# Kernel tuning notes

Hardware: AMD Instinct MI355X
Metric: run time of the kernel (lower is better)

## Reference

```python
import jax, jax.numpy as jnp
import numpy as np

B, C, T = 8, 16, 1024
DM, DI, DS, DR, DC, L = 128, 256, 16, 8, 4, 4  # d_model, d_inner=2*d_model, d_state, dt_rank=d_model//16, d_conv, n_layers


def setup_inputs() -> dict:
    key = jax.random.key(0)
    ks = jax.random.split(key, 12)
    n = jax.random.normal
    s = 0.02
    A_init = jnp.log(jnp.arange(1, DS + 1, dtype=jnp.float32))  # S4D-real init
    return {
        "eeg_input": n(ks[0], (B, C, T), jnp.float32),
        "Win": n(ks[1], (C, DM)) * s, "b_in": jnp.zeros((DM,)),
        "ln_w": jnp.ones((L, DM)), "ln_b": jnp.zeros((L, DM)),
        "in_w": n(ks[2], (L, 2, DM, 2 * DI)) * s,
        "conv_w": n(ks[3], (L, 2, DI, DC)) * s, "conv_b": jnp.zeros((L, 2, DI)),
        "xp_w": n(ks[4], (L, 2, DI, DR + 2 * DS)) * s,
        "dt_w": n(ks[5], (L, 2, DR, DI)) * s, "dt_b": jnp.full((L, 2, DI), -4.6),  # softplus(-4.6) ~ 0.01
        "A_log": jnp.tile(A_init, (L, 2, DI, 1)), "Dp": jnp.ones((L, 2, DI)),
        "out_w": n(ks[6], (L, 2, DI, DM)) * s, "out_b": jnp.zeros((L, 2, DM)),
        "cls_ln_w": jnp.ones((DM,)), "cls_ln_b": jnp.zeros((DM,)),
        "W1": n(ks[7], (DM, DM // 2)) * s, "b1": jnp.zeros((DM // 2,)),
        "W2": n(ks[8], (DM // 2, 1)) * s, "b2": jnp.zeros((1,)),
    }


def _ln(x, w, b):
    m = x.mean(-1, keepdims=True)
    v = ((x - m) ** 2).mean(-1, keepdims=True)
    return (x - m) * jax.lax.rsqrt(v + 1e-5) * w + b


def _mamba(u, in_w, conv_w, conv_b, xp_w, dt_w, dt_b, A_log, Dp, out_w, out_b):
    # u: (B, T, DM)
    xz = u @ in_w                              # (B, T, 2*DI)
    x, z = jnp.split(xz, 2, axis=-1)
    # causal depthwise conv along time
    xc = jnp.transpose(x, (0, 2, 1))           # (B, DI, T)
    xc = jax.lax.conv_general_dilated(
        xc, conv_w[:, None, :], (1,), [(DC - 1, 0)],
        dimension_numbers=("NCH", "OIH", "NCH"), feature_group_count=DI,
    ) + conv_b[None, :, None]
    x = jax.nn.silu(jnp.transpose(xc, (0, 2, 1)))  # (B, T, DI)
    xdbl = x @ xp_w                            # (B, T, DR+2*DS)
    dt, Bss, Css = jnp.split(xdbl, [DR, DR + DS], axis=-1)
    delta = jax.nn.softplus(dt @ dt_w + dt_b)  # (B, T, DI)
    A = -jnp.exp(A_log)                        # (DI, DS)
    dA = jnp.exp(delta[..., None] * A)                       # (B, T, DI, DS)
    dBu = delta[..., None] * Bss[:, :, None, :] * x[..., None]  # (B, T, DI, DS)

    def step(h, inputs):
        dA_t, dBu_t, C_t = inputs
        h = dA_t * h + dBu_t                   # (B, DI, DS)
        y = jnp.einsum("bds,bs->bd", h, C_t)
        return h, y

    h0 = jnp.zeros((u.shape[0], DI, DS), u.dtype)
    _, ys = jax.lax.scan(step, h0, (jnp.swapaxes(dA, 0, 1), jnp.swapaxes(dBu, 0, 1), jnp.swapaxes(Css, 0, 1)))
    y = jnp.swapaxes(ys, 0, 1) + Dp * x        # (B, T, DI)
    y = y * jax.nn.silu(z)
    return y @ out_w + out_b


def reference(eeg_input, Win, b_in, ln_w, ln_b, in_w, conv_w, conv_b, xp_w, dt_w, dt_b,
              A_log, Dp, out_w, out_b, cls_ln_w, cls_ln_b, W1, b1, W2, b2):
    h = jnp.transpose(eeg_input, (0, 2, 1)) @ Win + b_in  # (B, T, DM)
    for l in range(L):
        xn = _ln(h, ln_w[l], ln_b[l])
        yf = _mamba(xn, in_w[l, 0], conv_w[l, 0], conv_b[l, 0], xp_w[l, 0], dt_w[l, 0],
                    dt_b[l, 0], A_log[l, 0], Dp[l, 0], out_w[l, 0], out_b[l, 0])
        yb = _mamba(xn[:, ::-1], in_w[l, 1], conv_w[l, 1], conv_b[l, 1], xp_w[l, 1], dt_w[l, 1],
                    dt_b[l, 1], A_log[l, 1], Dp[l, 1], out_w[l, 1], out_b[l, 1])[:, ::-1]
        h = h + yf + yb  # residual; dropout is identity in eval
    pooled = h.mean(axis=1)                    # (B, DM)
    p = _ln(pooled, cls_ln_w, cls_ln_b)
    p = jax.nn.gelu(p @ W1 + b1)
    return p @ W2 + b2                         # (B, 1)
```

## Files before the change

### kernel.cpp

```cpp
#include <hip/hip_runtime.h>
#include <hip/hip_bf16.h>

#define NB 8
#define NC 16
#define NT 1024
#define DM 128
#define DI 256
#define DS 16
#define DR 8
#define DC 4
#define NL 4
#define NCHUNK 32
#define CL (NT / NCHUNK)
#define NCH 4096
#define PT (NB * NT)
#define CHW (PT * DI)
#define LOG2E 1.44269504088896f
#define LN2 0.69314718055995f

typedef __attribute__((ext_vector_type(8))) short short8;
typedef __attribute__((ext_vector_type(4))) float floatx4;

#define FLIP(m) (((m) & ~(NT - 1)) | ((NT - 1) - ((m) & (NT - 1))))

__global__ void wprep_k(const float* __restrict__ in_w, const float* __restrict__ xp_w,
                        const float* __restrict__ out_w, __hip_bfloat16* __restrict__ wT) {
    int i = blockIdx.x * 256 + threadIdx.x;
    if (i < 524288) {
        int g = i >> 16, rem = i & 65535, n = rem >> 7, k = rem & 127;
        wT[i] = __float2bfloat16(in_w[(size_t)g * 65536 + k * 512 + n]);
        return;
    }
    i -= 524288;
    if (i < 81920) {
        int g = i / 10240, rem = i % 10240, n = rem >> 8, k = rem & 255;
        wT[524288 + g * 10240 + n * 256 + k] = __float2bfloat16(xp_w[(size_t)g * 10240 + k * 40 + n]);
        return;
    }
    i -= 81920;
    if (i < 262144) {
        int g = i >> 15, rem = i & 32767, n = rem >> 8, k = rem & 255;
        wT[606208 + g * 32768 + n * 256 + k] = __float2bfloat16(out_w[(size_t)g * 32768 + k * 128 + n]);
    }
}

__global__ void embed_k(const float* __restrict__ eeg, const float* __restrict__ Win,
                        const float* __restrict__ b_in, float* __restrict__ h) {
    int g = blockIdx.x * 256 + threadIdx.x;
    int m = g & 127;
    int t = (g >> 7) & 1023;
    int b = g >> 17;
    float acc = b_in[m];
#pragma unroll
    for (int c = 0; c < NC; c++)
        acc += eeg[(b * NC + c) * NT + t] * Win[c * DM + m];
    h[g] = acc;
}

__global__ void lnadd_k(float* __restrict__ hbuf, const float* __restrict__ ytmp,
                        const float* __restrict__ w, const float* __restrict__ b,
                        __hip_bfloat16* __restrict__ xn, int doAdd) {
    int lane = threadIdx.x & 63;
    int row = (blockIdx.x * 256 + threadIdx.x) >> 6;
    float* hr = hbuf + (size_t)row * DM;
    float v0 = hr[lane], v1 = hr[lane + 64];
    if (doAdd) {
        const float* y0 = ytmp + (size_t)row * DM;
        const float* y1 = ytmp + (size_t)PT * DM + (size_t)FLIP(row) * DM;
        v0 += y0[lane] + y1[lane];
        v1 += y0[lane + 64] + y1[lane + 64];
        hr[lane] = v0;
        hr[lane + 64] = v1;
    }
    float s = v0 + v1, s2 = v0 * v0 + v1 * v1;
#pragma unroll
    for (int o = 1; o < 64; o <<= 1) {
        s += __shfl_xor(s, o);
        s2 += __shfl_xor(s2, o);
    }
    float mean = s * (1.f / 128.f);
    float var = s2 * (1.f / 128.f) - mean * mean;
    float rs = rsqrtf(var + 1e-5f);
    xn[(size_t)row * DM + lane]      = __float2bfloat16((v0 - mean) * rs * w[lane] + b[lane]);
    xn[(size_t)row * DM + lane + 64] = __float2bfloat16((v1 - mean) * rs * w[lane + 64] + b[lane + 64]);
}

__global__ __launch_bounds__(256) void mgemm_in_k(
    const __hip_bfloat16* __restrict__ A,
    const __hip_bfloat16* __restrict__ Wt, size_t wStr,
    __hip_bfloat16* __restrict__ O0, __hip_bfloat16* __restrict__ O1) {
    __shared__ __align__(16) __hip_bfloat16 As[64][40];
    __shared__ __align__(16) __hip_bfloat16 Bs[64][40];
    int z = blockIdx.z;
    Wt += (size_t)z * wStr;
    O0 += (size_t)z * CHW;
    O1 += (size_t)z * CHW;
    int m0 = blockIdx.x * 64, n0 = blockIdx.y * 64;
    int tid = threadIdx.x;
    int lane = tid & 63, w = tid >> 6;
    int wm = w >> 1, wn = w & 1;
    int lr = lane & 15, lh = lane >> 4;
    int rowL = tid >> 2, cc = tid & 3;
    floatx4 acc[2][2] = {};
    for (int k0 = 0; k0 < DM; k0 += 32) {
        int am = m0 + rowL;
        if (z) am = FLIP(am);
        *(float4*)&As[rowL][cc * 8] = *(const float4*)&A[(size_t)am * DM + k0 + cc * 8];
        *(float4*)&Bs[rowL][cc * 8] = *(const float4*)&Wt[(size_t)(n0 + rowL) * DM + k0 + cc * 8];
        __syncthreads();
        short8 a0 = *(const short8*)&As[wm * 32 + lr][lh * 8];
        short8 a1 = *(const short8*)&As[wm * 32 + 16 + lr][lh * 8];
        short8 b0 = *(const short8*)&Bs[wn * 32 + lr][lh * 8];
        short8 b1 = *(const short8*)&Bs[wn * 32 + 16 + lr][lh * 8];
        acc[0][0] = __builtin_amdgcn_mfma_f32_16x16x32_bf16(a0, b0, acc[0][0], 0, 0, 0);
        acc[1][0] = __builtin_amdgcn_mfma_f32_16x16x32_bf16(a1, b0, acc[1][0], 0, 0, 0);
        acc[0][1] = __builtin_amdgcn_mfma_f32_16x16x32_bf16(a0, b1, acc[0][1], 0, 0, 0);
        acc[1][1] = __builtin_amdgcn_mfma_f32_16x16x32_bf16(a1, b1, acc[1][1], 0, 0, 0);
        __syncthreads();
    }
#pragma unroll
    for (int mf = 0; mf < 2; mf++)
#pragma unroll
        for (int nf = 0; nf < 2; nf++)
#pragma unroll
            for (int r = 0; r < 4; r++) {
                int row = m0 + wm * 32 + mf * 16 + lh * 4 + r;
                int col = n0 + wn * 32 + nf * 16 + lr;
                __hip_bfloat16 v = __float2bfloat16(acc[mf][nf][r]);
                if (col < DI) O0[(size_t)row * DI + col] = v;
                else O1[(size_t)row * DI + col - DI] = v;
            }
}

__global__ __launch_bounds__(256) void mgemm_out_k(
    const __hip_bfloat16* __restrict__ A,
    const __hip_bfloat16* __restrict__ Wt, size_t wStr,
    const float* __restrict__ bias,
    float* __restrict__ O) {
    __shared__ __align__(16) __hip_bfloat16 As[64][40];
    __shared__ __align__(16) __hip_bfloat16 Bs[64][40];
    int z = blockIdx.z;
    A += (size_t)z * CHW;
    Wt += (size_t)z * wStr;
    bias += z * DM;
    O += (size_t)z * PT * DM;
    int m0 = blockIdx.x * 64, n0 = blockIdx.y * 64;
    int tid = threadIdx.x;
    int lane = tid & 63, w = tid >> 6;
    int wm = w >> 1, wn = w & 1;
    int lr = lane & 15, lh = lane >> 4;
    int rowL = tid >> 2, cc = tid & 3;
    floatx4 acc[2][2] = {};
    for (int k0 = 0; k0 < DI; k0 += 32) {
        *(float4*)&As[rowL][cc * 8] = *(const float4*)&A[(size_t)(m0 + rowL) * DI + k0 + cc * 8];
        *(float4*)&Bs[rowL][cc * 8] = *(const float4*)&Wt[(size_t)(n0 + rowL) * DI + k0 + cc * 8];
        __syncthreads();
        short8 a0 = *(const short8*)&As[wm * 32 + lr][lh * 8];
        short8 a1 = *(const short8*)&As[wm * 32 + 16 + lr][lh * 8];
        short8 b0 = *(const short8*)&Bs[wn * 32 + lr][lh * 8];
        short8 b1 = *(const short8*)&Bs[wn * 32 + 16 + lr][lh * 8];
        acc[0][0] = __builtin_amdgcn_mfma_f32_16x16x32_bf16(a0, b0, acc[0][0], 0, 0, 0);
        acc[1][0] = __builtin_amdgcn_mfma_f32_16x16x32_bf16(a1, b0, acc[1][0], 0, 0, 0);
        acc[0][1] = __builtin_amdgcn_mfma_f32_16x16x32_bf16(a0, b1, acc[0][1], 0, 0, 0);
        acc[1][1] = __builtin_amdgcn_mfma_f32_16x16x32_bf16(a1, b1, acc[1][1], 0, 0, 0);
        __syncthreads();
    }
#pragma unroll
    for (int mf = 0; mf < 2; mf++)
#pragma unroll
        for (int nf = 0; nf < 2; nf++)
#pragma unroll
            for (int r = 0; r < 4; r++) {
                int row = m0 + wm * 32 + mf * 16 + lh * 4 + r;
                int col = n0 + wn * 32 + nf * 16 + lr;
                O[(size_t)row * DM + col] = acc[mf][nf][r] + bias[col];
            }
}

__global__ __launch_bounds__(256) void xpgemm_k(
    const __hip_bfloat16* __restrict__ xpre,
    const __hip_bfloat16* __restrict__ Wt, size_t wStr,
    const float* __restrict__ cw, const float* __restrict__ cb,
    float* __restrict__ xdbl, __hip_bfloat16* __restrict__ xsil) {
    __shared__ __align__(16) __hip_bfloat16 As[64][40];
    __shared__ __align__(16) __hip_bfloat16 Bs[64][40];
    int z = blockIdx.z;
    const __hip_bfloat16* xp = xpre + (size_t)z * CHW;
    const __hip_bfloat16* wt = Wt + (size_t)z * wStr;
    const float* cwz = cw + z * DI * DC;
    const float* cbz = cb + z * DI;
    float* xd = xdbl + (size_t)z * PT * 40;
    __hip_bfloat16* xsz = xsil + (size_t)z * CHW;
    int m0 = blockIdx.x * 64;
    int tid = threadIdx.x;
    int lane = tid & 63, w = tid >> 6;
    int wm = w >> 1, wn = w & 1;
    int lr = lane & 15, lh = lane >> 4;
    int rowL = tid >> 2, cc = tid & 3;
    int m = m0 + rowL;
    int tloc = m & (NT - 1);
    floatx4 acc[2][2] = {};
    for (int k0 = 0; k0 < DI; k0 += 32) {
        int d0 = k0 + cc * 8;
        float a8[8];
#pragma unroll
        for (int jj = 0; jj < 8; jj++) a8[jj] = cbz[d0 + jj];
#pragma unroll
        for (int j = 0; j < DC; j++) {
            if (tloc - 3 + j >= 0) {
                const __hip_bfloat16* src = &xp[(size_t)(m - 3 + j) * DI + d0];
#pragma unroll
                for (int jj = 0; jj < 8; jj++)
                    a8[jj] += __bfloat162float(src[jj]) * cwz[(d0 + jj) * DC + j];
            }
        }
        __align__(16) __hip_bfloat16 h8[8];
#pragma unroll
        for (int jj = 0; jj < 8; jj++) {
            float v = a8[jj];
            v = v / (1.f + exp2f(-LOG2E * v));
            h8[jj] = __float2bfloat16(v);
        }
        *(float4*)&As[rowL][cc * 8] = *(const float4*)h8;
        *(float4*)&xsz[(size_t)m * DI + d0] = *(const float4*)h8;
        float4 bv = {0.f, 0.f, 0.f, 0.f};
        if (rowL < 40) bv = *(const float4*)&wt[(size_t)rowL * DI + k0 + cc * 8];
        *(float4*)&Bs[rowL][cc * 8] = bv;
        __syncthreads();
        short8 a0 = *(const short8*)&As[wm * 32 + lr][lh * 8];
        short8 a1 = *(const short8*)&As[wm * 32 + 16 + lr][lh * 8];
        short8 b0 = *(const short8*)&Bs[wn * 32 + lr][lh * 8];
        short8 b1 = *(const short8*)&Bs[wn * 32 + 16 + lr][lh * 8];
        acc[0][0] = __builtin_amdgcn_mfma_f32_16x16x32_bf16(a0, b0, acc[0][0], 0, 0, 0);
        acc[1][0] = __builtin_amdgcn_mfma_f32_16x16x32_bf16(a1, b0, acc[1][0], 0, 0, 0);
        acc[0][1] = __builtin_amdgcn_mfma_f32_16x16x32_bf16(a0, b1, acc[0][1], 0, 0, 0);
        acc[1][1] = __builtin_amdgcn_mfma_f32_16x16x32_bf16(a1, b1, acc[1][1], 0, 0, 0);
        __syncthreads();
    }
#pragma unroll
    for (int mf = 0; mf < 2; mf++)
#pragma unroll
        for (int nf = 0; nf < 2; nf++)
#pragma unroll
            for (int r = 0; r < 4; r++) {
                int row = m0 + wm * 32 + mf * 16 + lh * 4 + r;
                int col = wn * 32 + nf * 16 + lr;
                if (col < 40) xd[(size_t)row * 40 + col] = acc[mf][nf][r];
            }
}

__global__ __launch_bounds__(256) void scan1_k(
    const __hip_bfloat16* __restrict__ xsil, const float* __restrict__ xdbl,
    const float* __restrict__ dt_w, const float* __restrict__ dt_b,
    const float* __restrict__ A_log,
    __hip_bfloat16* __restrict__ deltab,
    float* __restrict__ smryA, float* __restrict__ smryH) {
    int cblk = blockIdx.y;
    int chan0 = blockIdx.x * 64;
    int rb = chan0 >> 8;
    int d0 = chan0 & 255;
    int r = chan0 >> 11;
    int tid = threadIdx.x;
    int ch = tid >> 2, sg = tid & 3;
    int t0 = cblk * CL;
    __shared__ uint x_s[CL * 32];
    __shared__ float bc_s[CL * 40];
    __shared__ __hip_bfloat16 del_s[CL][64];
    const uint* gx = (const uint*)(xsil + (size_t)rb * NT * DI + (size_t)t0 * DI + d0);
#pragma unroll
    for (int k = 0; k < 4; k++) {
        int e = tid + k * 256;
        x_s[e] = gx[(e >> 5) * 128 + (e & 31)];
    }
    const float* gxd = xdbl + (size_t)rb * NT * 40 + (size_t)t0 * 40;
#pragma unroll
    for (int k = 0; k < 5; k++) {
        int e = tid + k * 256;
        bc_s[e] = gxd[e];
    }
    __syncthreads();
    {
        int dd = tid & 63, ttb = tid >> 6;
        const float* dwr = dt_w + r * DR * DI + d0 + dd;
        float dwv[8];
#pragma unroll
        for (int j = 0; j < 8; j++) dwv[j] = dwr[j * DI];
        float dtb = dt_b[r * DI + d0 + dd];
#pragma unroll
        for (int q = 0; q < 8; q++) {
            int tt = ttb + q * 4;
            float4 q0 = *(const float4*)&bc_s[tt * 40];
            float4 q1 = *(const float4*)&bc_s[tt * 40 + 4];
            float acc = dtb + q0.x * dwv[0] + q0.y * dwv[1] + q0.z * dwv[2] + q0.w * dwv[3]
                            + q1.x * dwv[4] + q1.y * dwv[5] + q1.z * dwv[6] + q1.w * dwv[7];
            float sp = fmaxf(acc, 0.f) + LN2 * __log2f(1.f + exp2f(-LOG2E * fabsf(acc)));
            del_s[tt][dd] = __float2bfloat16(sp);
        }
    }
    __syncthreads();
    float Av2[4], hs[4] = {0.f, 0.f, 0.f, 0.f};
    float dlsum = 0.f;
#pragma unroll
    for (int i = 0; i < 4; i++)
        Av2[i] = -__expf(A_log[(r * DI + d0 + ch) * DS + sg * 4 + i]) * LOG2E;
    const __hip_bfloat16* xb = (const __hip_bfloat16*)x_s;
#pragma unroll 4
    for (int tt = 0; tt < CL; tt++) {
        float dl = __bfloat162float(del_s[tt][ch]);
        float xv = __bfloat162float(xb[tt * 64 + ch]);
        float u = dl * xv;
        dlsum += dl;
        float bb[4];
        *(float4*)bb = *(const float4*)&bc_s[tt * 40 + DR + sg * 4];
#pragma unroll
        for (int i = 0; i < 4; i++) {
            float dA = exp2f(dl * Av2[i]);
            hs[i] = dA * hs[i] + u * bb[i];
        }
    }
    float ap[4];
#pragma unroll
    for (int i = 0; i < 4; i++) ap[i] = exp2f(dlsum * Av2[i]);
    uint* gdel = (uint*)(deltab + (size_t)rb * NT * DI + (size_t)t0 * DI + d0);
#pragma unroll
    for (int k = 0; k < 4; k++) {
        int e = tid + k * 256;
        gdel[(e >> 5) * 128 + (e & 31)] = ((const uint*)del_s)[e];
    }
    size_t so = ((size_t)cblk * NCH + chan0 + ch) * 16 + sg * 4;
    *(float4*)(smryA + so) = *(const float4*)ap;
    *(float4*)(smryH + so) = *(const float4*)hs;
}

__global__ void scanH_k(const float* __restrict__ smryA, const float* __restrict__ smryH,
                        float* __restrict__ h0) {
    int g = blockIdx.x * 256 + threadIdx.x;
    float hh = 0.f;
#pragma unroll
    for (int c = 0; c < NCHUNK; c++) {
        size_t o = (size_t)c * (NCH * 16) + g;
        h0[o] = hh;
        hh = smryA[o] * hh + smryH[o];
    }
}

__global__ __launch_bounds__(256) void scan2_k(
    const __hip_bfloat16* __restrict__ deltab, const __hip_bfloat16* __restrict__ xsil,
    const __hip_bfloat16* __restrict__ zb, const float* __restrict__ xdbl,
    const float* __restrict__ A_log, const float* __restrict__ Dp,
    const float* __restrict__ h0, __hip_bfloat16* __restrict__ y) {
    int cblk = blockIdx.y;
    int chan0 = blockIdx.x * 64;
    int rb = chan0 >> 8;
    int d0 = chan0 & 255;
    int r = chan0 >> 11;
    int tid = threadIdx.x;
    int ch = tid >> 2, sg = tid & 3;
    int t0 = cblk * CL;
    __shared__ uint del_s[CL * 32], x_s[CL * 32], z_s[CL * 32];
    __shared__ float bc_s[CL * 32];
    __shared__ __hip_bfloat16 y_s[CL][64];
    size_t tilebase = (size_t)rb * NT * DI + (size_t)t0 * DI + d0;
    const uint* gd = (const uint*)(deltab + tilebase);
    const uint* gx = (const uint*)(xsil + tilebase);
    const uint* gz = (const uint*)(zb + tilebase);
#pragma unroll
    for (int k = 0; k < 4; k++) {
        int e = tid + k * 256;
        int a = (e >> 5) * 128 + (e & 31);
        del_s[e] = gd[a];
        x_s[e] = gx[a];
        z_s[e] = gz[a];
    }
    const float* gxd = xdbl + (size_t)rb * NT * 40 + (size_t)t0 * 40;
#pragma unroll
    for (int k = 0; k < 4; k++) {
        int e = tid + k * 256;
        bc_s[e] = gxd[(e >> 5) * 40 + DR + (e & 31)];
    }
    float Av2[4], hs[4];
#pragma unroll
    for (int i = 0; i < 4; i++)
        Av2[i] = -__expf(A_log[(r * DI + d0 + ch) * DS + sg * 4 + i]) * LOG2E;
    float4 hv = *(const float4*)(h0 + ((size_t)cblk * NCH + chan0 + ch) * 16 + sg * 4);
    *(float4*)hs = hv;
    float Dv = Dp[r * DI + d0 + ch];
    __syncthreads();
    const __hip_bfloat16* db = (const __hip_bfloat16*)del_s;
    const __hip_bfloat16* xb = (const __hip_bfloat16*)x_s;
    const __hip_bfloat16* zbb2 = (const __hip_bfloat16*)z_s;
#pragma unroll 4
    for (int tt = 0; tt < CL; tt++) {
        float dl = __bfloat162float(db[tt * 64 + ch]);
        float xv = __bfloat162float(xb[tt * 64 + ch]);
        float u = dl * xv;
        float bb[4], cv[4];
        *(float4*)bb = *(const float4*)&bc_s[tt * 32 + sg * 4];
        *(float4*)cv = *(const float4*)&bc_s[tt * 32 + 16 + sg * 4];
        float py = 0.f;
#pragma unroll
        for (int i = 0; i < 4; i++) {
            float dA = exp2f(dl * Av2[i]);
            hs[i] = dA * hs[i] + u * bb[i];
            py += hs[i] * cv[i];
        }
        py += __shfl_xor(py, 1);
        py += __shfl_xor(py, 2);
        if (sg == 0) {
            float zv = __bfloat162float(zbb2[tt * 64 + ch]);
            float sig = 1.f / (1.f + exp2f(-LOG2E * zv));
            y_s[tt][ch] = __float2bfloat16((py + Dv * xv) * (zv * sig));
        }
    }
    __syncthreads();
    uint* gy = (uint*)(y + tilebase);
#pragma unroll
    for (int k = 0; k < 4; k++) {
        int e = tid + k * 256;
        gy[(e >> 5) * 128 + (e & 31)] = ((const uint*)y_s)[e];
    }
}

__global__ void pooladd_k(const float* __restrict__ h, const float* __restrict__ ytmp,
                          float* __restrict__ partial) {
    int b = blockIdx.x, tc = blockIdx.y, m = threadIdx.x;
    float acc = 0.f;
    for (int i = 0; i < 64; i++) {
        int row = b * NT + tc * 64 + i;
        acc += h[(size_t)row * DM + m] + ytmp[(size_t)row * DM + m]
             + ytmp[(size_t)PT * DM + (size_t)FLIP(row) * DM + m];
    }
    partial[(b * 16 + tc) * DM + m] = acc;
}

__global__ __launch_bounds__(128) void cls_k(
    const float* __restrict__ partial, const float* __restrict__ lw,
    const float* __restrict__ lb, const float* __restrict__ W1,
    const float* __restrict__ b1, const float* __restrict__ W2,
    const float* __restrict__ b2, float* __restrict__ out) {
    __shared__ float red[128], pbuf[128], qbuf[64];
    int b = blockIdx.x, i = threadIdx.x;
    float v = 0.f;
    for (int tc = 0; tc < 16; tc++) v += partial[(b * 16 + tc) * DM + i];
    v *= (1.f / NT);
    red[i] = v;
    __syncthreads();
    for (int o = 64; o > 0; o >>= 1) { if (i < o) red[i] += red[i + o]; __syncthreads(); }
    float mean = red[0] * (1.f / 128.f);
    __syncthreads();
    red[i] = (v - mean) * (v - mean);
    __syncthreads();
    for (int o = 64; o > 0; o >>= 1) { if (i < o) red[i] += red[i + o]; __syncthreads(); }
    float var = red[0] * (1.f / 128.f);
    float p = (v - mean) * rsqrtf(var + 1e-5f) * lw[i] + lb[i];
    pbuf[i] = p;
    __syncthreads();
    if (i < 64) {
        float acc = b1[i];
        for (int k = 0; k < 128; k++) acc += pbuf[k] * W1[k * 64 + i];
        float x = acc;
        float tt = tanhf(0.7978845608028654f * (x + 0.044715f * x * x * x));
        qbuf[i] = 0.5f * x * (1.f + tt);
    }
    __syncthreads();
    if (i == 0) {
        float acc = b2[0];
        for (int k = 0; k < 64; k++) acc += qbuf[k] * W2[k];
        out[b] = acc;
    }
}

extern "C" void kernel_launch(void* const* d_in, const int* in_sizes, int n_in,
                              void* d_out, int out_size, void* d_ws, size_t ws_size,
                              hipStream_t stream) {
    const float* eeg    = (const float*)d_in[0];
    const float* Win    = (const float*)d_in[1];
    const float* b_in   = (const float*)d_in[2];
    const float* ln_w   = (const float*)d_in[3];
    const float* ln_b   = (const float*)d_in[4];
    const float* in_w   = (const float*)d_in[5];
    const float* conv_w = (const float*)d_in[6];
    const float* conv_b = (const float*)d_in[7];
    const float* xp_w   = (const float*)d_in[8];
    const float* dt_w   = (const float*)d_in[9];
    const float* dt_b   = (const float*)d_in[10];
    const float* A_log  = (const float*)d_in[11];
    const float* Dp     = (const float*)d_in[12];
    const float* out_w  = (const float*)d_in[13];
    const float* out_b  = (const float*)d_in[14];
    const float* clw    = (const float*)d_in[15];
    const float* clb    = (const float*)d_in[16];
    const float* W1     = (const float*)d_in[17];
    const float* b1     = (const float*)d_in[18];
    const float* W2     = (const float*)d_in[19];
    const float* b2     = (const float*)d_in[20];
    float* out = (float*)d_out;

    float* ws = (float*)d_ws;
    float* h      = ws;
    float* xdbl   = h + PT * DM;
    float* smryA  = xdbl + 2 * PT * 40;
    float* smryH  = smryA + NCHUNK * NCH * 16;
    float* h0buf  = smryH + NCHUNK * NCH * 16;
    float* partial = h0buf + NCHUNK * NCH * 16;
    float* ytmp   = smryA;
    __hip_bfloat16* xnb    = (__hip_bfloat16*)(partial + 16384);
    __hip_bfloat16* xpreb  = xnb + PT * DM;
    __hip_bfloat16* zbb    = xpreb + 2 * CHW;
    __hip_bfloat16* xsilb  = zbb + 2 * CHW;
    __hip_bfloat16* deltab = xsilb + 2 * CHW;
    __hip_bfloat16* yb     = deltab + 2 * CHW;
    __hip_bfloat16* wT     = yb + 2 * CHW;
    __hip_bfloat16* wTin   = wT;
    __hip_bfloat16* wTxp   = wT + 524288;
    __hip_bfloat16* wTout  = wT + 606208;

    wprep_k<<<3392, 256, 0, stream>>>(in_w, xp_w, out_w, wT);
    embed_k<<<PT * DM / 256, 256, 0, stream>>>(eeg, Win, b_in, h);

    for (int l = 0; l < NL; l++) {
        lnadd_k<<<PT / 4, 256, 0, stream>>>(h, ytmp, ln_w + l * DM, ln_b + l * DM, xnb, l > 0);
        mgemm_in_k<<<dim3(PT / 64, 8, 2), 256, 0, stream>>>(
            xnb, wTin + (size_t)l * 2 * 65536, 65536, xpreb, zbb);
        xpgemm_k<<<dim3(PT / 64, 1, 2), 256, 0, stream>>>(
            xpreb, wTxp + (size_t)l * 2 * 10240, 10240,
            conv_w + (size_t)l * 2 * DI * DC, conv_b + (size_t)l * 2 * DI,
            xdbl, xsilb);
        scan1_k<<<dim3(NCH / 64, NCHUNK), 256, 0, stream>>>(
            xsilb, xdbl, dt_w + (size_t)l * 2 * DR * DI, dt_b + (size_t)l * 2 * DI,
            A_log + (size_t)l * 2 * DI * DS, deltab, smryA, smryH);
        scanH_k<<<NCH * 16 / 256, 256, 0, stream>>>(smryA, smryH, h0buf);
        scan2_k<<<dim3(NCH / 64, NCHUNK), 256, 0, stream>>>(
            deltab, xsilb, zbb, xdbl, A_log + (size_t)l * 2 * DI * DS,
            Dp + (size_t)l * 2 * DI, h0buf, yb);
        mgemm_out_k<<<dim3(PT / 64, 2, 2), 256, 0, stream>>>(
            yb, wTout + (size_t)l * 2 * 32768, 32768,
            out_b + (size_t)l * 2 * DM, ytmp);
    }

    pooladd_k<<<dim3(NB, 16), DM, 0, stream>>>(h, ytmp, partial);
    cls_k<<<NB, DM, 0, stream>>>(partial, clw, clb, W1, b1, W2, b2, out);
}
```

Measured before the change: 476.2 us.

## Replace second chunk scan pass with elementwise carry-in correction kernel

The first scan pass now also produces each chunk's local output, computed from a zero initial state, together with the running delta sum. Both are packed as bf16 plus fp16 into one word per element. The second sequential scan kernel is replaced by an elementwise kernel that adds the carried-in state contribution, sum over s of C*h0*exp(cumdelta*A). It also applies the D skip term and the SiLU gate there. The -exp(A_log) table is precomputed once, and the delta buffer is no longer written. The aim is to remove a full second recurrence pass and its shared-memory staging, at the cost of 16 extra exponentials per output and reduced precision in the stored partial output and cumulative delta.

```diff
diff --git a/kernel.cpp b/kernel.cpp
--- a/kernel.cpp
+++ b/kernel.cpp
@@ -1,5 +1,6 @@
 #include <hip/hip_runtime.h>
 #include <hip/hip_bf16.h>
+#include <hip/hip_fp16.h>
 
 #define NB 8
 #define NC 16
@@ -42,6 +43,11 @@
         int g = i >> 15, rem = i & 32767, n = rem >> 8, k = rem & 255;
         wT[606208 + g * 32768 + n * 256 + k] = __float2bfloat16(out_w[(size_t)g * 32768 + k * 128 + n]);
     }
+}
+
+__global__ void avprep_k(const float* __restrict__ A_log, float* __restrict__ avtab) {
+    int i = blockIdx.x * 256 + threadIdx.x;
+    avtab[i] = -__expf(A_log[i]) * LOG2E;
 }
 
 __global__ void embed_k(const float* __restrict__ eeg, const float* __restrict__ Win,
@@ -252,8 +258,8 @@
 __global__ __launch_bounds__(256) void scan1_k(
     const __hip_bfloat16* __restrict__ xsil, const float* __restrict__ xdbl,
     const float* __restrict__ dt_w, const float* __restrict__ dt_b,
-    const float* __restrict__ A_log,
-    __hip_bfloat16* __restrict__ deltab,
+    const float* __restrict__ avtab,
+    uint* __restrict__ pycum,
     float* __restrict__ smryA, float* __restrict__ smryH) {
     int cblk = blockIdx.y;
     int chan0 = blockIdx.x * 64;
@@ -266,6 +272,7 @@
     __shared__ uint x_s[CL * 32];
     __shared__ float bc_s[CL * 40];
     __shared__ __hip_bfloat16 del_s[CL][64];
+    __shared__ uint pc_s[CL * 64];
     const uint* gx = (const uint*)(xsil + (size_t)rb * NT * DI + (size_t)t0 * DI + d0);
 #pragma unroll
     for (int k = 0; k < 4; k++) {
@@ -298,11 +305,9 @@
         }
     }
     __syncthreads();
-    float Av2[4], hs[4] = {0.f, 0.f, 0.f, 0.f};
+    float av[4], hs[4] = {0.f, 0.f, 0.f, 0.f};
+    *(float4*)av = *(const float4*)(avtab + ((size_t)r * DI + d0 + ch) * DS + sg * 4);
     float dlsum = 0.f;
-#pragma unroll
-    for (int i = 0; i < 4; i++)
-        Av2[i] = -__expf(A_log[(r * DI + d0 + ch) * DS + sg * 4 + i]) * LOG2E;
     const __hip_bfloat16* xb = (const __hip_bfloat16*)x_s;
 #pragma unroll 4
     for (int tt = 0; tt < CL; tt++) {
@@ -310,115 +315,85 @@
         float xv = __bfloat162float(xb[tt * 64 + ch]);
         float u = dl * xv;
         dlsum += dl;
-        float bb[4];
+        float bb[4], cv[4];
         *(float4*)bb = *(const float4*)&bc_s[tt * 40 + DR + sg * 4];
+        *(float4*)cv = *(const float4*)&bc_s[tt * 40 + DR + DS + sg * 4];
+        float py = 0.f;
 #pragma unroll
         for (int i = 0; i < 4; i++) {
-            float dA = exp2f(dl * Av2[i]);
-            hs[i] = dA * hs[i] + u * bb[i];
-        }
-    }
-    float ap[4];
-#pragma unroll
-    for (int i = 0; i < 4; i++) ap[i] = exp2f(dlsum * Av2[i]);
-    uint* gdel = (uint*)(deltab + (size_t)rb * NT * DI + (size_t)t0 * DI + d0);
-#pragma unroll
-    for (int k = 0; k < 4; k++) {
-        int e = tid + k * 256;
-        gdel[(e >> 5) * 128 + (e & 31)] = ((const uint*)del_s)[e];
-    }
-    size_t so = ((size_t)cblk * NCH + chan0 + ch) * 16 + sg * 4;
-    *(float4*)(smryA + so) = *(const float4*)ap;
-    *(float4*)(smryH + so) = *(const float4*)hs;
-}
-
-__global__ void scanH_k(const float* __restrict__ smryA, const float* __restrict__ smryH,
-                        float* __restrict__ h0) {
-    int g = blockIdx.x * 256 + threadIdx.x;
-    float hh = 0.f;
-#pragma unroll
-    for (int c = 0; c < NCHUNK; c++) {
-        size_t o = (size_t)c * (NCH * 16) + g;
-        h0[o] = hh;
-        hh = smryA[o] * hh + smryH[o];
-    }
-}
-
-__global__ __launch_bounds__(256) void scan2_k(
-    const __hip_bfloat16* __restrict__ deltab, const __hip_bfloat16* __restrict__ xsil,
-    const __hip_bfloat16* __restrict__ zb, const float* __restrict__ xdbl,
-    const float* __restrict__ A_log, const float* __restrict__ Dp,
-    const float* __restrict__ h0, __hip_bfloat16* __restrict__ y) {
-    int cblk = blockIdx.y;
-    int chan0 = blockIdx.x * 64;
-    int rb = chan0 >> 8;
-    int d0 = chan0 & 255;
-    int r = chan0 >> 11;
-    int tid = threadIdx.x;
-    int ch = tid >> 2, sg = tid & 3;
-    int t0 = cblk * CL;
-    __shared__ uint del_s[CL * 32], x_s[CL * 32], z_s[CL * 32];
-    __shared__ float bc_s[CL * 32];
-    __shared__ __hip_bfloat16 y_s[CL][64];
-    size_t tilebase = (size_t)rb * NT * DI + (size_t)t0 * DI + d0;
-    const uint* gd = (const uint*)(deltab + tilebase);
-    const uint* gx = (const uint*)(xsil + tilebase);
-    const uint* gz = (const uint*)(zb + tilebase);
-#pragma unroll
-    for (int k = 0; k < 4; k++) {
-        int e = tid + k * 256;
-        int a = (e >> 5) * 128 + (e & 31);
-        del_s[e] = gd[a];
-        x_s[e] = gx[a];
-        z_s[e] = gz[a];
-    }
-    const float* gxd = xdbl + (size_t)rb * NT * 40 + (size_t)t0 * 40;
-#pragma unroll
-    for (int k = 0; k < 4; k++) {
-        int e = tid + k * 256;
-        bc_s[e] = gxd[(e >> 5) * 40 + DR + (e & 31)];
-    }
-    float Av2[4], hs[4];
-#pragma unroll
-    for (int i = 0; i < 4; i++)
-        Av2[i] = -__expf(A_log[(r * DI + d0 + ch) * DS + sg * 4 + i]) * LOG2E;
-    float4 hv = *(const float4*)(h0 + ((size_t)cblk * NCH + chan0 + ch) * 16 + sg * 4);
-    *(float4*)hs = hv;
-    float Dv = Dp[r * DI + d0 + ch];
-    __syncthreads();
-    const __hip_bfloat16* db = (const __hip_bfloat16*)del_s;
-    const __hip_bfloat16* xb = (const __hip_bfloat16*)x_s;
-    const __hip_bfloat16* zbb2 = (const __hip_bfloat16*)z_s;
-#pragma unroll 4
-    for (int tt = 0; tt < CL; tt++) {
-        float dl = __bfloat162float(db[tt * 64 + ch]);
-        float xv = __bfloat162float(xb[tt * 64 + ch]);
-        float u = dl * xv;
-        float bb[4], cv[4];
-        *(float4*)bb = *(const float4*)&bc_s[tt * 32 + sg * 4];
-        *(float4*)cv = *(const float4*)&bc_s[tt * 32 + 16 + sg * 4];
-        float py = 0.f;
-#pragma unroll
-        for (int i = 0; i < 4; i++) {
-            float dA = exp2f(dl * Av2[i]);
+            float dA = exp2f(dl * av[i]);
             hs[i] = dA * hs[i] + u * bb[i];
             py += hs[i] * cv[i];
         }
         py += __shfl_xor(py, 1);
         py += __shfl_xor(py, 2);
         if (sg == 0) {
-            float zv = __bfloat162float(zbb2[tt * 64 + ch]);
-            float sig = 1.f / (1.f + exp2f(-LOG2E * zv));
-            y_s[tt][ch] = __float2bfloat16((py + Dv * xv) * (zv * sig));
+            __hip_bfloat16 pb = __float2bfloat16(py);
+            __half hc = __float2half(dlsum);
+            pc_s[tt * 64 + ch] = (uint)(*(ushort*)&pb) | ((uint)(*(ushort*)&hc) << 16);
         }
     }
-    __syncthreads();
-    uint* gy = (uint*)(y + tilebase);
-#pragma unroll
-    for (int k = 0; k < 4; k++) {
+    float ap[4];
+#pragma unroll
+    for (int i = 0; i < 4; i++) ap[i] = exp2f(dlsum * av[i]);
+    __syncthreads();
+    uint* gpc = pycum + (size_t)rb * NT * DI + (size_t)t0 * DI + d0;
+#pragma unroll
+    for (int k = 0; k < 8; k++) {
         int e = tid + k * 256;
-        gy[(e >> 5) * 128 + (e & 31)] = ((const uint*)y_s)[e];
-    }
+        gpc[(e >> 6) * DI + (e & 63)] = pc_s[e];
+    }
+    size_t so = ((size_t)cblk * NCH + chan0 + ch) * 16 + sg * 4;
+    *(float4*)(smryA + so) = *(const float4*)ap;
+    *(float4*)(smryH + so) = *(const float4*)hs;
+}
+
+__global__ void scanH_k(const float* __restrict__ smryA, const float* __restrict__ smryH,
+                        float* __restrict__ h0) {
+    int g = blockIdx.x * 256 + threadIdx.x;
+    float hh = 0.f;
+#pragma unroll
+    for (int c = 0; c < NCHUNK; c++) {
+        size_t o = (size_t)c * (NCH * 16) + g;
+        h0[o] = hh;
+        hh = smryA[o] * hh + smryH[o];
+    }
+}
+
+__global__ __launch_bounds__(256) void yfix_k(
+    const uint* __restrict__ pycum, const __hip_bfloat16* __restrict__ xsil,
+    const __hip_bfloat16* __restrict__ zb, const float* __restrict__ xdbl,
+    const float* __restrict__ avtab, const float* __restrict__ Dp,
+    const float* __restrict__ h0, __hip_bfloat16* __restrict__ y) {
+    int g = blockIdx.x * 256 + threadIdx.x;
+    int d = g & 255;
+    int t = (g >> 8) & (NT - 1);
+    int rb = g >> 18;
+    int r = g >> 21;
+    int cblk = t >> 5;
+    int chan = rb * 256 + d;
+    uint pc = pycum[g];
+    ushort plo = (ushort)pc, phi = (ushort)(pc >> 16);
+    float py = __bfloat162float(*(__hip_bfloat16*)&plo);
+    float cum = __half2float(*(__half*)&phi);
+    const float* av = avtab + ((size_t)r * DI + d) * DS;
+    const float* hp = h0 + ((size_t)cblk * NCH + chan) * 16;
+    const float* crow = xdbl + ((size_t)rb * NT + t) * 40 + DR + DS;
+    float c4[16], h4[16], a4[16];
+#pragma unroll
+    for (int q = 0; q < 4; q++) {
+        *(float4*)&c4[q * 4] = *(const float4*)(crow + q * 4);
+        *(float4*)&h4[q * 4] = *(const float4*)(hp + q * 4);
+        *(float4*)&a4[q * 4] = *(const float4*)(av + q * 4);
+    }
+    float corr = 0.f;
+#pragma unroll
+    for (int s = 0; s < 16; s++)
+        corr += c4[s] * h4[s] * exp2f(cum * a4[s]);
+    float xv = __bfloat162float(xsil[g]);
+    float zv = __bfloat162float(zb[g]);
+    float sig = 1.f / (1.f + exp2f(-LOG2E * zv));
+    y[g] = __float2bfloat16((py + corr + Dp[r * DI + d] * xv) * (zv * sig));
 }
 
 __global__ void pooladd_k(const float* __restrict__ h, const float* __restrict__ ytmp,
@@ -497,28 +472,31 @@
     float* out = (float*)d_out;
 
     float* ws = (float*)d_ws;
-    float* h      = ws;
-    float* xdbl   = h + PT * DM;
-    float* smryA  = xdbl + 2 * PT * 40;
-    float* smryH  = smryA + NCHUNK * NCH * 16;
-    float* h0buf  = smryH + NCHUNK * NCH * 16;
+    float* h       = ws;
+    float* xdbl    = h + PT * DM;
+    float* smryA   = xdbl + 2 * PT * 40;
+    float* smryH   = smryA + NCHUNK * NCH * 16;
+    float* h0buf   = smryH + NCHUNK * NCH * 16;
     float* partial = h0buf + NCHUNK * NCH * 16;
-    float* ytmp   = smryA;
-    __hip_bfloat16* xnb    = (__hip_bfloat16*)(partial + 16384);
+    float* avtab   = partial + 16384;
+    uint*  pycum   = (uint*)(avtab + 32768);
+    float* ytmp    = smryA;
+    __hip_bfloat16* xnb    = (__hip_bfloat16*)(pycum + 2 * CHW);
     __hip_bfloat16* xpreb  = xnb + PT * DM;
     __hip_bfloat16* zbb    = xpreb + 2 * CHW;
     __hip_bfloat16* xsilb  = zbb + 2 * CHW;
-    __hip_bfloat16* deltab = xsilb + 2 * CHW;
-    __hip_bfloat16* yb     = deltab + 2 * CHW;
-    __hip_bfloat16* wT     = yb + 2 * CHW;
+    __hip_bfloat16* wT     = xsilb + 2 * CHW;
     __hip_bfloat16* wTin   = wT;
     __hip_bfloat16* wTxp   = wT + 524288;
     __hip_bfloat16* wTout  = wT + 606208;
+    __hip_bfloat16* yb     = xpreb;
 
     wprep_k<<<3392, 256, 0, stream>>>(in_w, xp_w, out_w, wT);
+    avprep_k<<<128, 256, 0, stream>>>(A_log, avtab);
     embed_k<<<PT * DM / 256, 256, 0, stream>>>(eeg, Win, b_in, h);
 
     for (int l = 0; l < NL; l++) {
+        const float* avl = avtab + (size_t)l * 2 * DI * DS;
         lnadd_k<<<PT / 4, 256, 0, stream>>>(h, ytmp, ln_w + l * DM, ln_b + l * DM, xnb, l > 0);
         mgemm_in_k<<<dim3(PT / 64, 8, 2), 256, 0, stream>>>(
             xnb, wTin + (size_t)l * 2 * 65536, 65536, xpreb, zbb);
@@ -528,11 +506,10 @@
             xdbl, xsilb);
         scan1_k<<<dim3(NCH / 64, NCHUNK), 256, 0, stream>>>(
             xsilb, xdbl, dt_w + (size_t)l * 2 * DR * DI, dt_b + (size_t)l * 2 * DI,
-            A_log + (size_t)l * 2 * DI * DS, deltab, smryA, smryH);
+            avl, pycum, smryA, smryH);
         scanH_k<<<NCH * 16 / 256, 256, 0, stream>>>(smryA, smryH, h0buf);
-        scan2_k<<<dim3(NCH / 64, NCHUNK), 256, 0, stream>>>(
-            deltab, xsilb, zbb, xdbl, A_log + (size_t)l * 2 * DI * DS,
-            Dp + (size_t)l * 2 * DI, h0buf, yb);
+        yfix_k<<<2 * CHW / 256, 256, 0, stream>>>(
+            pycum, xsilb, zbb, xdbl, avl, Dp + (size_t)l * 2 * DI, h0buf, yb);
         mgemm_out_k<<<dim3(PT / 64, 2, 2), 256, 0, stream>>>(
             yb, wTout + (size_t)l * 2 * 32768, 32768,
             out_b + (size_t)l * 2 * DM, ytmp);
```

Measured after the change: 512.9 us. 1.08x slower.
